# Performance work log

Hardware: AMD Instinct MI355X
Metric: run time of the kernel (lower is better)

The kernel has to match this reference:

```python
import jax, jax.numpy as jnp
import numpy as np

N_NODES = 100000
N_EDGES = 3200000
N_GRAPHS = 128
F_IN, HID, N_CLS = 3, 64, 6


def setup_inputs() -> dict:
    key = jax.random.key(0)
    ks = jax.random.split(key, 9)
    x = jax.random.normal(ks[0], (N_NODES, F_IN), dtype=jnp.float32)
    edge_index = jax.random.randint(ks[1], (2, N_EDGES), 0, N_NODES, dtype=jnp.int32)
    batch = jnp.sort(jax.random.randint(ks[2], (N_NODES,), 0, N_GRAPHS, dtype=jnp.int32))
    # GCNConv weights (glorot-ish) and biases
    W1 = jax.random.normal(ks[3], (F_IN, HID), dtype=jnp.float32) / np.float32(np.sqrt(F_IN))
    b1 = jnp.zeros((HID,), dtype=jnp.float32)
    W2 = jax.random.normal(ks[4], (HID, HID), dtype=jnp.float32) / np.float32(np.sqrt(HID))
    b2 = jnp.zeros((HID,), dtype=jnp.float32)
    Wl = jax.random.normal(ks[5], (HID, N_CLS), dtype=jnp.float32) / np.float32(np.sqrt(HID))
    bl = jnp.zeros((N_CLS,), dtype=jnp.float32)
    return {"x": x, "edge_index": edge_index, "batch": batch,
            "W1": W1, "b1": b1, "W2": W2, "b2": b2, "Wl": Wl, "bl": bl}


def _gcn_forward(x, edge_index, batch, W1, b1, W2, b2, Wl, bl):
    n = x.shape[0]
    # add self-loops (PyG GCNConv default)
    loop = jnp.arange(n, dtype=edge_index.dtype)
    src = jnp.concatenate([edge_index[0], loop])
    dst = jnp.concatenate([edge_index[1], loop])
    # symmetric normalization D^{-1/2} (A+I) D^{-1/2}
    deg = jax.ops.segment_sum(jnp.ones_like(dst, dtype=x.dtype), dst, num_segments=n)
    dis = jax.lax.rsqrt(jnp.maximum(deg, 1.0))
    norm = dis[src] * dis[dst]  # [E+N]

    def conv(h, W, b):
        h = h @ W                                   # [N, out]
        msg = h[src] * norm[:, None]                # gather + scale
        agg = jax.ops.segment_sum(msg, dst, num_segments=n)  # scatter-add
        return agg + b

    h = jax.nn.relu(conv(x, W1, b1))
    h = jax.nn.relu(conv(h, W2, b2))
    # global mean pool over graphs
    ones = jnp.ones((n,), dtype=h.dtype)
    cnt = jax.ops.segment_sum(ones, batch, num_segments=N_GRAPHS)
    pooled = jax.ops.segment_sum(h, batch, num_segments=N_GRAPHS) / jnp.maximum(cnt, 1.0)[:, None]
    logits = pooled @ Wl + bl
    return jax.nn.log_softmax(logits, axis=1)


def reference(x, edge_index, batch, W1, b1, W2, b2, Wl, bl):
    return _gcn_forward(x, edge_index, batch, W1, b1, W2, b2, Wl, bl)
```

## Files before the change

### kernel.cpp

```cpp
#include <hip/hip_runtime.h>
#include <math.h>

#define NGRAPH 128
#define NPB 128
#define CAPB 6144
#define MMN 16
#define TILEA 16384
#define EPTA 16


__device__ inline unsigned char f2fp8(float f) {
    float a = fabsf(f);
    unsigned s = (__float_as_uint(f) >> 31) << 7;
    if (!(a > 0.f)) return (unsigned char)s;
    if (a >= 448.f) return (unsigned char)(s | 0x7e);
    int e = (int)(__float_as_uint(a) >> 23) - 127;
    if (e < -6) e = -6;
    float sc = __uint_as_float((unsigned)(130 - e) << 23);
    int q = (int)rintf(a * sc);
    if (q >= 16) { e += 1; q = 8; }
    if (q <= 0) return (unsigned char)s;
    unsigned expb, man;
    if (q < 8) { expb = 0; man = (unsigned)q; }
    else { expb = (unsigned)(e + 7); man = (unsigned)(q - 8); }
    return (unsigned char)(s | (expb << 3) | man);
}

typedef float v2f __attribute__((ext_vector_type(2)));

__device__ inline void fp8x4_dec(unsigned u, float* o) {
#pragma unroll
    for (int k = 0; k < 4; ++k) {
        unsigned b = (u >> (8 * k)) & 0xffu;
        unsigned bits = ((b & 0x80u) << 24) | ((b & 0x7fu) << 20);
        o[k] = __uint_as_float(bits) * 0x1p+120f;
    }
}

__device__ inline void acc16(uint4 u, float w, v2f* a) {
#if __has_builtin(__builtin_amdgcn_cvt_pk_f32_fp8)
    v2f ws; ws.x = w; ws.y = w;
    a[0] += __builtin_amdgcn_cvt_pk_f32_fp8(u.x, false) * ws;
    a[1] += __builtin_amdgcn_cvt_pk_f32_fp8(u.x, true)  * ws;
    a[2] += __builtin_amdgcn_cvt_pk_f32_fp8(u.y, false) * ws;
    a[3] += __builtin_amdgcn_cvt_pk_f32_fp8(u.y, true)  * ws;
    a[4] += __builtin_amdgcn_cvt_pk_f32_fp8(u.z, false) * ws;
    a[5] += __builtin_amdgcn_cvt_pk_f32_fp8(u.z, true)  * ws;
    a[6] += __builtin_amdgcn_cvt_pk_f32_fp8(u.w, false) * ws;
    a[7] += __builtin_amdgcn_cvt_pk_f32_fp8(u.w, true)  * ws;
#else
    float* af = (float*)a;
    unsigned uu[4] = {u.x, u.y, u.z, u.w};
#pragma unroll
    for (int q = 0; q < 4; ++q) {
        float d[4]; fp8x4_dec(uu[q], d);
#pragma unroll
        for (int k = 0; k < 4; ++k) af[q * 4 + k] += d[k] * w;
    }
#endif
}


__global__ void init_k(int* __restrict__ cursorF, float* __restrict__ pooled, int NBF) {
    int i = blockIdx.x * blockDim.x + threadIdx.x;
    if (i < NBF) cursorF[i] = i * CAPB;
    if (i < NGRAPH * 64) pooled[i] = 0.0f;
}


__global__ __launch_bounds__(1024) void binA_k(const int* __restrict__ src,
        const int* __restrict__ dst, int* cursorF, unsigned* __restrict__ binned,
        int E, int NBF) {
    __shared__ int lh[1024];
    __shared__ int startv[1024];
    __shared__ int gdelta[1024];
    __shared__ unsigned lout[TILEA];
    int tid = threadIdx.x;
    lh[tid] = 0;
    __syncthreads();
    int base = blockIdx.x * TILEA;
    int d[EPTA];
    int s[EPTA];
#pragma unroll
    for (int u = 0; u < EPTA; ++u) {
        int e = base + tid + u * 1024;
        d[u] = (e < E) ? dst[e] : -1;
        s[u] = (e < E) ? src[e] : 0;
    }
#pragma unroll
    for (int u = 0; u < EPTA; ++u)
        if (d[u] >= 0) atomicAdd(&lh[d[u] >> 7], 1);
    __syncthreads();
    if (tid <= NBF) startv[tid] = (tid == 0) ? 0 : lh[tid - 1];
    __syncthreads();
    for (int off = 1; off <= NBF; off <<= 1) {
        int v = 0;
        if (tid <= NBF && tid >= off) v = startv[tid - off];
        __syncthreads();
        if (tid <= NBF && tid >= off) startv[tid] += v;
        __syncthreads();
    }
    if (tid < NBF) {
        int cnt = lh[tid];
        int g = cnt ? atomicAdd(&cursorF[tid], cnt) : 0;
        gdelta[tid] = g - startv[tid];
        lh[tid] = startv[tid];
    }
    __syncthreads();
#pragma unroll
    for (int u = 0; u < EPTA; ++u) {
        if (d[u] >= 0) {
            int p = atomicAdd(&lh[d[u] >> 7], 1);
            lout[p] = (unsigned)s[u] | ((unsigned)(d[u] & (NPB - 1)) << 17);
        }
    }
    __syncthreads();
    int wv = tid >> 6, ln = tid & 63;
    for (int bkt = wv; bkt < NBF; bkt += 16) {
        int ls = startv[bkt], le = lh[bkt];
        int gd = gdelta[bkt];
        for (int i = ls + ln; i < le; i += 64)
            binned[gd + i] = lout[i];
    }
}


__global__ __launch_bounds__(256) void reorder_k(unsigned* __restrict__ binned,
        const int* __restrict__ cursorF, int* __restrict__ nodebeg,
        int* __restrict__ nodeend, float* __restrict__ dis,
        const float* __restrict__ x, float* __restrict__ xs, int n) {
    __shared__ int hist[NPB + 1];
    __shared__ int startv[NPB + 1];
    __shared__ unsigned lout[CAPB];
    int tid = threadIdx.x;
    int b = blockIdx.x;
    int beg = b * CAPB, end = cursorF[b];
    int total = end - beg;
    if (tid <= NPB) hist[tid] = 0;
    __syncthreads();
    for (int i = beg + tid; i < end; i += 256)
        atomicAdd(&hist[binned[i] >> 17], 1);
    __syncthreads();
    if (tid < NPB) startv[tid + 1] = hist[tid];
    if (tid == 0) startv[0] = 0;
    __syncthreads();
    for (int off = 1; off <= NPB; off <<= 1) {
        int v = 0;
        if (tid <= NPB && tid >= off) v = startv[tid - off];
        __syncthreads();
        if (tid <= NPB && tid >= off) startv[tid] += v;
        __syncthreads();
    }
    if (tid < NPB) hist[tid] = startv[tid];
    __syncthreads();
    for (int i = beg + tid; i < end; i += 256) {
        unsigned r = binned[i];
        int p = atomicAdd(&hist[r >> 17], 1);
        lout[p] = r & 0x1FFFFu;
    }
    __syncthreads();
    for (int jj = tid; jj < total; jj += 256)
        binned[beg + jj] = lout[jj];
    int node0 = b * NPB;
    if (tid < NPB) {
        int node = node0 + tid;
        if (node < n) {
            nodebeg[node] = beg + startv[tid];
            nodeend[node] = beg + startv[tid + 1];
            int deg = startv[tid + 1] - startv[tid];
            float d = rsqrtf((float)deg + 1.0f);
            dis[node] = d;
            xs[node * 3]     = x[node * 3] * d;
            xs[node * 3 + 1] = x[node * 3 + 1] * d;
            xs[node * 3 + 2] = x[node * 3 + 2] * d;
        }
    }
}


__global__ __launch_bounds__(256) void mm12_k(const float* __restrict__ xs,
        const int* __restrict__ nodebeg, const int* __restrict__ nodeend,
        const int* __restrict__ csr, const float* __restrict__ dis,
        const float* __restrict__ W1, const float* __restrict__ b1,
        const float* __restrict__ W2, unsigned char* __restrict__ tb, int n) {
    __shared__ __attribute__((aligned(16))) float hrow[4][64];
    __shared__ float4 ytile[MMN];
    int tid = threadIdx.x;
    int j = tid & 63;

    float w1r0 = W1[j], w1r1 = W1[64 + j], w1r2 = W1[128 + j], bbr = b1[j];
    float wreg[64];
#pragma unroll
    for (int k = 0; k < 64; ++k) wreg[k] = W2[k * 64 + j];

    int ns = tid >> 4;
    int el = tid & 15;
    int gnode = blockIdx.x * MMN + ns;
    float a0 = 0.f, a1 = 0.f, a2 = 0.f;
    float dn = 0.f;
    int b = 0, e = 0;
    if (gnode < n) {
        dn = dis[gnode];
        b = nodebeg[gnode];
        e = nodeend[gnode];
    }
    for (int i = b + el; i < e; i += 64) {
        int i1 = i + 16, i2 = i + 32, i3 = i + 48;
        int s0 = csr[i];
        int s1 = (i1 < e) ? csr[i1] : s0;
        int s2 = (i2 < e) ? csr[i2] : s0;
        int s3 = (i3 < e) ? csr[i3] : s0;
        float m1 = (i1 < e) ? 1.f : 0.f;
        float m2 = (i2 < e) ? 1.f : 0.f;
        float m3 = (i3 < e) ? 1.f : 0.f;
        float p0 = xs[s0 * 3], p1 = xs[s0 * 3 + 1], p2 = xs[s0 * 3 + 2];
        float q0 = xs[s1 * 3], q1 = xs[s1 * 3 + 1], q2 = xs[s1 * 3 + 2];
        float r0 = xs[s2 * 3], r1 = xs[s2 * 3 + 1], r2 = xs[s2 * 3 + 2];
        float t0 = xs[s3 * 3], t1 = xs[s3 * 3 + 1], t2 = xs[s3 * 3 + 2];
        a0 += p0 + q0 * m1 + r0 * m2 + t0 * m3;
        a1 += p1 + q1 * m1 + r1 * m2 + t1 * m3;
        a2 += p2 + q2 * m1 + r2 * m2 + t2 * m3;
    }
#pragma unroll
    for (int off = 1; off <= 8; off <<= 1) {
        a0 += __shfl_xor(a0, off);
        a1 += __shfl_xor(a1, off);
        a2 += __shfl_xor(a2, off);
    }
    if (el == 0 && gnode < n) {
        ytile[ns] = make_float4(dn * (a0 + xs[gnode * 3]),
                                dn * (a1 + xs[gnode * 3 + 1]),
                                dn * (a2 + xs[gnode * 3 + 2]), dn);
    }
    __syncthreads();

    int nl = tid >> 6;
    for (int it = 0; it < MMN / 4; ++it) {
        int slot = it * 4 + nl;
        int node = blockIdx.x * MMN + slot;
        float4 yv = ytile[slot];
        float h = fmaxf(yv.x * w1r0 + yv.y * w1r1 + yv.z * w1r2 + bbr, 0.0f);
        hrow[nl][j] = h;
        __builtin_amdgcn_wave_barrier();
        float acc = 0.0f;
#pragma unroll
        for (int k = 0; k < 64; k += 4) {
            float4 h4 = *(const float4*)&hrow[nl][k];
            acc += h4.x * wreg[k + 0];
            acc += h4.y * wreg[k + 1];
            acc += h4.z * wreg[k + 2];
            acc += h4.w * wreg[k + 3];
        }
        if (node < n) tb[node * 64 + j] = f2fp8(acc * yv.w);
        __builtin_amdgcn_wave_barrier();
    }
}


__global__ __launch_bounds__(256) void gather2_k(const unsigned char* __restrict__ tb,
        const float* __restrict__ b2, const int* __restrict__ nodebeg,
        const int* __restrict__ nodeend, const int* __restrict__ csr,
        const float* __restrict__ dis, const int* __restrict__ batch,
        float* __restrict__ pooled, int n) {
    __shared__ float pacc[4][64];
    __shared__ int gbase;
    int tid = threadIdx.x;
    ((float*)pacc)[tid] = 0.f;
    int node0 = blockIdx.x * 8;
    if (tid == 0) gbase = batch[node0 < n ? node0 : (n - 1)];
    __syncthreads();

    int g = blockIdx.x * blockDim.x + tid;
    int node = g >> 5;
    int l32 = tid & 31;
    int c4 = l32 & 3, esub = l32 >> 2;
    if (node < n) {
        const uint4* t16 = (const uint4*)tb;
        float dn = dis[node];
        int b = nodebeg[node], e = nodeend[node];
        v2f av[8];
#pragma unroll
        for (int k = 0; k < 8; ++k) { av[k].x = 0.f; av[k].y = 0.f; }
        for (int i = b; i < e + 1; i += 64) {
            int i0 = i + esub;
            int s0 = (i0      < e) ? csr[i0]      : node;
            int s1 = (i0 + 8  < e) ? csr[i0 + 8]  : node;
            int s2 = (i0 + 16 < e) ? csr[i0 + 16] : node;
            int s3 = (i0 + 24 < e) ? csr[i0 + 24] : node;
            int s4 = (i0 + 32 < e) ? csr[i0 + 32] : node;
            int s5 = (i0 + 40 < e) ? csr[i0 + 40] : node;
            int s6 = (i0 + 48 < e) ? csr[i0 + 48] : node;
            int s7 = (i0 + 56 < e) ? csr[i0 + 56] : node;
            uint4 u0 = t16[s0 * 4 + c4];
            uint4 u1 = t16[s1 * 4 + c4];
            uint4 u2 = t16[s2 * 4 + c4];
            uint4 u3 = t16[s3 * 4 + c4];
            uint4 u4 = t16[s4 * 4 + c4];
            uint4 u5 = t16[s5 * 4 + c4];
            uint4 u6 = t16[s6 * 4 + c4];
            uint4 u7 = t16[s7 * 4 + c4];
            acc16(u0, (i0      <= e) ? 1.f : 0.f, av);
            acc16(u1, (i0 + 8  <= e) ? 1.f : 0.f, av);
            acc16(u2, (i0 + 16 <= e) ? 1.f : 0.f, av);
            acc16(u3, (i0 + 24 <= e) ? 1.f : 0.f, av);
            acc16(u4, (i0 + 32 <= e) ? 1.f : 0.f, av);
            acc16(u5, (i0 + 40 <= e) ? 1.f : 0.f, av);
            acc16(u6, (i0 + 48 <= e) ? 1.f : 0.f, av);
            acc16(u7, (i0 + 56 <= e) ? 1.f : 0.f, av);
        }
        float* a = (float*)av;
        {
            bool hi = (esub & 1) != 0;
#pragma unroll
            for (int t = 0; t < 8; ++t) {
                float send = hi ? a[t] : a[8 + t];
                float r = __shfl_xor(send, 4);
                a[t] = (hi ? a[8 + t] : a[t]) + r;
            }
        }
        {
            bool hi = (esub & 2) != 0;
#pragma unroll
            for (int t = 0; t < 4; ++t) {
                float send = hi ? a[t] : a[4 + t];
                float r = __shfl_xor(send, 8);
                a[t] = (hi ? a[4 + t] : a[t]) + r;
            }
        }
        {
            bool hi = (esub & 4) != 0;
#pragma unroll
            for (int t = 0; t < 2; ++t) {
                float send = hi ? a[t] : a[2 + t];
                float r = __shfl_xor(send, 16);
                a[t] = (hi ? a[2 + t] : a[t]) + r;
            }
        }
        int cb = ((esub & 1) << 3) | ((esub & 2) << 1) | ((esub & 4) >> 1);
        int ch = c4 * 16 + cb;
        v2f bv = *(const v2f*)&b2[ch];
        float v0 = fmaxf(dn * a[0] + bv.x, 0.f);
        float v1 = fmaxf(dn * a[1] + bv.y, 0.f);
        int gid = batch[node];
        int bin = gid - gbase;
        if (bin < 4) {
            atomicAdd(&pacc[bin][ch], v0);
            atomicAdd(&pacc[bin][ch + 1], v1);
        } else {
            atomicAdd(&pooled[gid * 64 + ch], v0);
            atomicAdd(&pooled[gid * 64 + ch + 1], v1);
        }
    }
    __syncthreads();
    int fbin = tid >> 6, fch = tid & 63;
    float fv = pacc[fbin][fch];
    if (fv != 0.f) atomicAdd(&pooled[(gbase + fbin) * 64 + fch], fv);
}


__device__ inline int lower_bound_i(const int* a, int n, int key) {
    int lo = 0, hi = n;
    while (lo < hi) {
        int mid = (lo + hi) >> 1;
        if (a[mid] < key) lo = mid + 1; else hi = mid;
    }
    return lo;
}

__global__ void head_k(const float* __restrict__ pooled, const int* __restrict__ batch,
                       const float* __restrict__ Wl, const float* __restrict__ bl,
                       float* __restrict__ out, int n) {
    int g = blockIdx.x, t = threadIdx.x;
    __shared__ float p[64];
    __shared__ float logit[8];
    int start = lower_bound_i(batch, n, g);
    int end   = lower_bound_i(batch, n, g + 1);
    float cnt = fmaxf((float)(end - start), 1.0f);
    p[t] = pooled[g * 64 + t] / cnt;
    __syncthreads();
    if (t < 6) {
        float a = bl[t];
        for (int k = 0; k < 64; ++k) a += p[k] * Wl[k * 6 + t];
        logit[t] = a;
    }
    __syncthreads();
    if (t == 0) {
        float m = logit[0];
        for (int j = 1; j < 6; ++j) m = fmaxf(m, logit[j]);
        float s = 0.0f;
        for (int j = 0; j < 6; ++j) s += expf(logit[j] - m);
        float lse = m + logf(s);
        for (int j = 0; j < 6; ++j) out[g * 6 + j] = logit[j] - lse;
    }
}


extern "C" void kernel_launch(void* const* d_in, const int* in_sizes, int n_in,
                              void* d_out, int out_size, void* d_ws, size_t ws_size,
                              hipStream_t stream) {
    const float* x     = (const float*)d_in[0];
    const int*   ei    = (const int*)d_in[1];
    const int*   batch = (const int*)d_in[2];
    const float* W1    = (const float*)d_in[3];
    const float* b1    = (const float*)d_in[4];
    const float* W2    = (const float*)d_in[5];
    const float* b2    = (const float*)d_in[6];
    const float* Wl    = (const float*)d_in[7];
    const float* bl    = (const float*)d_in[8];

    int n = in_sizes[0] / 3;
    int E = in_sizes[1] / 2;
    const int* src = ei;
    const int* dst = ei + E;

    int NBF = (n + NPB - 1) / NPB;
    int GA = (E + TILEA - 1) / TILEA;

    char* ws = (char*)d_ws;
    size_t o = 0;
    auto alloc = [&](size_t bytes) -> void* {
        void* p = ws + o;
        o += (bytes + 255) & ~(size_t)255;
        return p;
    };
    int*      cursorF = (int*)alloc((size_t)NBF * 4);
    float*    dis     = (float*)alloc((size_t)n * 4);
    int*      nodebeg = (int*)alloc((size_t)n * 4);
    int*      nodeend = (int*)alloc((size_t)n * 4);
    float*    xs      = (float*)alloc((size_t)n * 3 * 4);
    float*    pooled  = (float*)alloc((size_t)NGRAPH * 64 * 4);
    unsigned* binned  = (unsigned*)alloc((size_t)NBF * CAPB * 4);
    unsigned char* tb = (unsigned char*)alloc((size_t)n * 64);
    float*    out = (float*)d_out;

    int initN = NGRAPH * 64;
    init_k<<<(initN + 255) / 256, 256, 0, stream>>>(cursorF, pooled, NBF);
    binA_k<<<GA, 1024, 0, stream>>>(src, dst, cursorF, binned, E, NBF);
    reorder_k<<<NBF, 256, 0, stream>>>(binned, cursorF, nodebeg, nodeend, dis, x, xs, n);

    mm12_k<<<(n + MMN - 1) / MMN, 256, 0, stream>>>(xs, nodebeg, nodeend,
            (const int*)binned, dis, W1, b1, W2, tb, n);
    gather2_k<<<(n * 32 + 255) / 256, 256, 0, stream>>>(tb, b2, nodebeg, nodeend,
            (const int*)binned, dis, batch, pooled, n);

    head_k<<<NGRAPH, 64, 0, stream>>>(pooled, batch, Wl, bl, out, n);
}
```

Before: 219.0 us.

## Split fp8 layer-2 features into two halves and gather each in a separate pass

mm12_k now writes the fp8 transformed features into two 32-channel arrays instead of one 64-channel array. gather2_k is launched twice, once per half, with 16 lanes per node and a channel offset for bias and pooling. The aim is to shrink each pass's random-gather working set (3.2 MB instead of 6.4 MB) so it fits better in cache, at the cost of reading the CSR twice and an extra launch. reorder_k also stages its bin slice in LDS once instead of reading global memory twice.

```diff
diff --git a/kernel.cpp b/kernel.cpp
--- a/kernel.cpp
+++ b/kernel.cpp
@@ -131,15 +131,17 @@
         const float* __restrict__ x, float* __restrict__ xs, int n) {
     __shared__ int hist[NPB + 1];
     __shared__ int startv[NPB + 1];
+    __shared__ unsigned lin[CAPB];
     __shared__ unsigned lout[CAPB];
     int tid = threadIdx.x;
     int b = blockIdx.x;
     int beg = b * CAPB, end = cursorF[b];
     int total = end - beg;
     if (tid <= NPB) hist[tid] = 0;
-    __syncthreads();
-    for (int i = beg + tid; i < end; i += 256)
-        atomicAdd(&hist[binned[i] >> 17], 1);
+    for (int i = tid; i < total; i += 256) lin[i] = binned[beg + i];
+    __syncthreads();
+    for (int i = tid; i < total; i += 256)
+        atomicAdd(&hist[lin[i] >> 17], 1);
     __syncthreads();
     if (tid < NPB) startv[tid + 1] = hist[tid];
     if (tid == 0) startv[0] = 0;
@@ -153,8 +155,8 @@
     }
     if (tid < NPB) hist[tid] = startv[tid];
     __syncthreads();
-    for (int i = beg + tid; i < end; i += 256) {
-        unsigned r = binned[i];
+    for (int i = tid; i < total; i += 256) {
+        unsigned r = lin[i];
         int p = atomicAdd(&hist[r >> 17], 1);
         lout[p] = r & 0x1FFFFu;
     }
@@ -182,7 +184,8 @@
         const int* __restrict__ nodebeg, const int* __restrict__ nodeend,
         const int* __restrict__ csr, const float* __restrict__ dis,
         const float* __restrict__ W1, const float* __restrict__ b1,
-        const float* __restrict__ W2, unsigned char* __restrict__ tb, int n) {
+        const float* __restrict__ W2, unsigned char* __restrict__ tbA,
+        unsigned char* __restrict__ tbB, int n) {
     __shared__ __attribute__((aligned(16))) float hrow[4][64];
     __shared__ float4 ytile[MMN];
     int tid = threadIdx.x;
@@ -251,31 +254,35 @@
             acc += h4.z * wreg[k + 2];
             acc += h4.w * wreg[k + 3];
         }
-        if (node < n) tb[node * 64 + j] = f2fp8(acc * yv.w);
+        if (node < n) {
+            unsigned char val = f2fp8(acc * yv.w);
+            if (j < 32) tbA[node * 32 + j] = val;
+            else        tbB[node * 32 + (j - 32)] = val;
+        }
         __builtin_amdgcn_wave_barrier();
     }
 }
 
 
-__global__ __launch_bounds__(256) void gather2_k(const unsigned char* __restrict__ tb,
+__global__ __launch_bounds__(256) void gather2_k(const unsigned char* __restrict__ tbH,
         const float* __restrict__ b2, const int* __restrict__ nodebeg,
         const int* __restrict__ nodeend, const int* __restrict__ csr,
         const float* __restrict__ dis, const int* __restrict__ batch,
-        float* __restrict__ pooled, int n) {
-    __shared__ float pacc[4][64];
+        float* __restrict__ pooled, int poolOff, int n) {
+    __shared__ float pacc[4][32];
     __shared__ int gbase;
     int tid = threadIdx.x;
-    ((float*)pacc)[tid] = 0.f;
-    int node0 = blockIdx.x * 8;
+    if (tid < 128) ((float*)pacc)[tid] = 0.f;
+    int node0 = blockIdx.x * 16;
     if (tid == 0) gbase = batch[node0 < n ? node0 : (n - 1)];
     __syncthreads();
 
     int g = blockIdx.x * blockDim.x + tid;
-    int node = g >> 5;
-    int l32 = tid & 31;
-    int c4 = l32 & 3, esub = l32 >> 2;
+    int node = g >> 4;
+    int l16 = tid & 15;
+    int c4 = l16 & 1, esub = l16 >> 1;
     if (node < n) {
-        const uint4* t16 = (const uint4*)tb;
+        const uint4* t16 = (const uint4*)tbH;
         float dn = dis[node];
         int b = nodebeg[node], e = nodeend[node];
         v2f av[8];
@@ -291,14 +298,14 @@
             int s5 = (i0 + 40 < e) ? csr[i0 + 40] : node;
             int s6 = (i0 + 48 < e) ? csr[i0 + 48] : node;
             int s7 = (i0 + 56 < e) ? csr[i0 + 56] : node;
-            uint4 u0 = t16[s0 * 4 + c4];
-            uint4 u1 = t16[s1 * 4 + c4];
-            uint4 u2 = t16[s2 * 4 + c4];
-            uint4 u3 = t16[s3 * 4 + c4];
-            uint4 u4 = t16[s4 * 4 + c4];
-            uint4 u5 = t16[s5 * 4 + c4];
-            uint4 u6 = t16[s6 * 4 + c4];
-            uint4 u7 = t16[s7 * 4 + c4];
+            uint4 u0 = t16[s0 * 2 + c4];
+            uint4 u1 = t16[s1 * 2 + c4];
+            uint4 u2 = t16[s2 * 2 + c4];
+            uint4 u3 = t16[s3 * 2 + c4];
+            uint4 u4 = t16[s4 * 2 + c4];
+            uint4 u5 = t16[s5 * 2 + c4];
+            uint4 u6 = t16[s6 * 2 + c4];
+            uint4 u7 = t16[s7 * 2 + c4];
             acc16(u0, (i0      <= e) ? 1.f : 0.f, av);
             acc16(u1, (i0 + 8  <= e) ? 1.f : 0.f, av);
             acc16(u2, (i0 + 16 <= e) ? 1.f : 0.f, av);
@@ -314,7 +321,7 @@
 #pragma unroll
             for (int t = 0; t < 8; ++t) {
                 float send = hi ? a[t] : a[8 + t];
-                float r = __shfl_xor(send, 4);
+                float r = __shfl_xor(send, 2);
                 a[t] = (hi ? a[8 + t] : a[t]) + r;
             }
         }
@@ -323,7 +330,7 @@
 #pragma unroll
             for (int t = 0; t < 4; ++t) {
                 float send = hi ? a[t] : a[4 + t];
-                float r = __shfl_xor(send, 8);
+                float r = __shfl_xor(send, 4);
                 a[t] = (hi ? a[4 + t] : a[t]) + r;
             }
         }
@@ -332,13 +339,13 @@
 #pragma unroll
             for (int t = 0; t < 2; ++t) {
                 float send = hi ? a[t] : a[2 + t];
-                float r = __shfl_xor(send, 16);
+                float r = __shfl_xor(send, 8);
                 a[t] = (hi ? a[2 + t] : a[t]) + r;
             }
         }
         int cb = ((esub & 1) << 3) | ((esub & 2) << 1) | ((esub & 4) >> 1);
         int ch = c4 * 16 + cb;
-        v2f bv = *(const v2f*)&b2[ch];
+        v2f bv = *(const v2f*)&b2[poolOff + ch];
         float v0 = fmaxf(dn * a[0] + bv.x, 0.f);
         float v1 = fmaxf(dn * a[1] + bv.y, 0.f);
         int gid = batch[node];
@@ -347,14 +354,16 @@
             atomicAdd(&pacc[bin][ch], v0);
             atomicAdd(&pacc[bin][ch + 1], v1);
         } else {
-            atomicAdd(&pooled[gid * 64 + ch], v0);
-            atomicAdd(&pooled[gid * 64 + ch + 1], v1);
-        }
-    }
-    __syncthreads();
-    int fbin = tid >> 6, fch = tid & 63;
-    float fv = pacc[fbin][fch];
-    if (fv != 0.f) atomicAdd(&pooled[(gbase + fbin) * 64 + fch], fv);
+            atomicAdd(&pooled[gid * 64 + poolOff + ch], v0);
+            atomicAdd(&pooled[gid * 64 + poolOff + ch + 1], v1);
+        }
+    }
+    __syncthreads();
+    if (tid < 128) {
+        int fbin = tid >> 5, fch = tid & 31;
+        float fv = pacc[fbin][fch];
+        if (fv != 0.f) atomicAdd(&pooled[(gbase + fbin) * 64 + poolOff + fch], fv);
+    }
 }
 
 
@@ -430,7 +439,8 @@
     float*    xs      = (float*)alloc((size_t)n * 3 * 4);
     float*    pooled  = (float*)alloc((size_t)NGRAPH * 64 * 4);
     unsigned* binned  = (unsigned*)alloc((size_t)NBF * CAPB * 4);
-    unsigned char* tb = (unsigned char*)alloc((size_t)n * 64);
+    unsigned char* tbA = (unsigned char*)alloc((size_t)n * 32);
+    unsigned char* tbB = (unsigned char*)alloc((size_t)n * 32);
     float*    out = (float*)d_out;
 
     int initN = NGRAPH * 64;
@@ -439,9 +449,13 @@
     reorder_k<<<NBF, 256, 0, stream>>>(binned, cursorF, nodebeg, nodeend, dis, x, xs, n);
 
     mm12_k<<<(n + MMN - 1) / MMN, 256, 0, stream>>>(xs, nodebeg, nodeend,
-            (const int*)binned, dis, W1, b1, W2, tb, n);
-    gather2_k<<<(n * 32 + 255) / 256, 256, 0, stream>>>(tb, b2, nodebeg, nodeend,
-            (const int*)binned, dis, batch, pooled, n);
+            (const int*)binned, dis, W1, b1, W2, tbA, tbB, n);
+
+    int GG = (n * 16 + 255) / 256;
+    gather2_k<<<GG, 256, 0, stream>>>(tbA, b2, nodebeg, nodeend,
+            (const int*)binned, dis, batch, pooled, 0, n);
+    gather2_k<<<GG, 256, 0, stream>>>(tbB, b2, nodebeg, nodeend,
+            (const int*)binned, dis, batch, pooled, 32, n);
 
     head_k<<<NGRAPH, 64, 0, stream>>>(pooled, batch, Wl, bl, out, n);
 }
```

New measurement: 226.7 us. 3.5% more time.
